# Kernel tuning notes

Hardware: AMD Instinct MI355X
Metric: run time of the kernel (lower is better)

## Reference

```python
import jax, jax.numpy as jnp
import numpy as np

N_NODES = 16384
N_EDGES = 262144
N_GRAPHS = 64
COLORS = 16
EMB = 256
HEADS = 8
FFN = 1024
LAYERS = 4
LMAX = 320


def _ln(x, g, b, eps=1e-5):
    m = x.mean(-1, keepdims=True)
    v = x.var(-1, keepdims=True)
    return (x - m) * jax.lax.rsqrt(v + eps) * g + b


def setup_inputs() -> dict:
    key = jax.random.key(0)
    ks = iter(jax.random.split(key, 64))
    s = 0.05
    def rn(shape):
        return jax.random.normal(next(ks), shape, jnp.float32) * s
    # 64 graphs: 32 with 192 nodes, 32 with 320 nodes -> total 16384, L_max=320
    lengths = np.concatenate([np.full(32, 192, np.int64), np.full(32, 320, np.int64)])
    batches = jnp.asarray(np.concatenate([[0], np.cumsum(lengths)]).astype(np.int32))
    x = jax.random.normal(next(ks), (N_NODES, COLORS), jnp.float32)
    edge_index = jax.random.randint(next(ks), (2, N_EDGES), 0, N_NODES, jnp.int32)
    inp = dict(
        x=x, edge_index=edge_index, batches=batches, L_max=LMAX,
        sW0=rn((COLORS, EMB)), sWn0=rn((COLORS, EMB)), sb0=jnp.zeros(EMB),
        sW1=rn((EMB, EMB)), sWn1=rn((EMB, EMB)), sb1=jnp.zeros(EMB),
        sW2=rn((EMB, EMB)), sWn2=rn((EMB, EMB)), sb2=jnp.zeros(EMB),
        Wq=rn((LAYERS, EMB, EMB)), Wk=rn((LAYERS, EMB, EMB)), Wv=rn((LAYERS, EMB, EMB)),
        bq=jnp.zeros((LAYERS, EMB)), bk=jnp.zeros((LAYERS, EMB)), bv=jnp.zeros((LAYERS, EMB)),
        Wo=rn((LAYERS, EMB, EMB)), bo=jnp.zeros((LAYERS, EMB)),
        ln1g=jnp.ones((LAYERS, EMB)), ln1b=jnp.zeros((LAYERS, EMB)),
        ln2g=jnp.ones((LAYERS, EMB)), ln2b=jnp.zeros((LAYERS, EMB)),
        W1=rn((LAYERS, EMB, FFN)), b1=jnp.zeros((LAYERS, FFN)),
        W2=rn((LAYERS, FFN, EMB)), b2=jnp.zeros((LAYERS, EMB)),
    )
    return inp


def reference(x, edge_index, batches, L_max,
              sW0, sWn0, sb0, sW1, sWn1, sb1, sW2, sWn2, sb2,
              Wq, Wk, Wv, bq, bk, bv, Wo, bo,
              ln1g, ln1b, ln2g, ln2b, W1, b1, W2, b2):
    N = x.shape[0]
    src, dst = edge_index[0], edge_index[1]
    deg = jnp.maximum(
        jax.ops.segment_sum(jnp.ones(src.shape[0], x.dtype), dst, num_segments=N), 1.0
    )[:, None]

    def sage(h, Ws, Wn, b, act):
        agg = jax.ops.segment_sum(h[src], dst, num_segments=N) / deg  # mean neighbor agg
        h2 = h @ Ws + agg @ Wn + b
        return jax.nn.relu(h2) if act else h2

    z = sage(x, sW0, sWn0, sb0, True)
    z = sage(z, sW1, sWn1, sb1, True)
    z = sage(z, sW2, sWn2, sb2, False)

    # pack_and_pad (intended semantics): seq-first [L_max, n_graphs, D] + key padding mask
    nG = batches.shape[0] - 1
    lengths = batches[1:] - batches[:-1]
    ids = jnp.arange(N)
    seg = jnp.searchsorted(batches, ids, side='right') - 1  # graph id per node
    pos = ids - batches[seg]                                 # position within graph
    D = z.shape[1]
    h = jnp.zeros((L_max, nG, D), z.dtype).at[pos, seg].set(z)
    pad = jnp.arange(L_max)[None, :] >= lengths[:, None]     # [nG, L_max], True = padded

    H = HEADS
    dh = D // H
    scale = 1.0 / np.sqrt(dh).astype(np.float32)
    for l in range(Wq.shape[0]):
        L, Bg = h.shape[0], h.shape[1]
        q = (h @ Wq[l] + bq[l]).reshape(L, Bg, H, dh)
        k = (h @ Wk[l] + bk[l]).reshape(L, Bg, H, dh)
        v = (h @ Wv[l] + bv[l]).reshape(L, Bg, H, dh)
        sc = jnp.einsum('lbhd,mbhd->bhlm', q, k) * scale
        sc = jnp.where(pad[:, None, None, :], -1e9, sc)
        a = jax.nn.softmax(sc, axis=-1)
        o = jnp.einsum('bhlm,mbhd->lbhd', a, v).reshape(L, Bg, D) @ Wo[l] + bo[l]
        h = _ln(h + o, ln1g[l], ln1b[l])
        ff = jax.nn.relu(h @ W1[l] + b1[l]) @ W2[l] + b2[l]
        h = _ln(h + ff, ln2g[l], ln2b[l])
    return h
```

## Files before the change

### kernel.cpp

```cpp
#include <hip/hip_runtime.h>
#include <hip/hip_bf16.h>
#include <math.h>

#define NN  16384
#define NE  262144
#define NG  64
#define CIN 16
#define DD  256
#define NHD 8
#define DHD 32
#define DFF 1024
#define NLY 4
#define LM  320
#define NR  (LM*NG)
#define QS  768
#define QKW 512

typedef __attribute__((ext_vector_type(8))) short bf16x8;
typedef __attribute__((ext_vector_type(4))) float f32x4;

__device__ __forceinline__ unsigned short f2bf(float f) {
    union { __hip_bfloat16 h; unsigned short u; } cv;
    cv.h = __float2bfloat16(f);
    return cv.u;
}
__device__ __forceinline__ float bf2f(unsigned short u) {
    return __uint_as_float((unsigned int)u << 16);
}
__device__ __forceinline__ void gl_lds16(const unsigned short* g, unsigned short* l) {
    __builtin_amdgcn_global_load_lds(
        (const __attribute__((address_space(1))) unsigned int*)g,
        (__attribute__((address_space(3))) unsigned int*)l, 16, 0, 0);
}

__global__ void zero_ws_kernel(uint4* __restrict__ hb, int n16, int* __restrict__ counts) {
    int i = blockIdx.x * 256 + threadIdx.x;
    if (i < n16) hb[i] = (uint4){0u, 0u, 0u, 0u};
    if (i < NN) counts[i] = 0;
}

__global__ __launch_bounds__(256) void prep_all_kernel(
    const float* __restrict__ Wq, const float* __restrict__ Wk, const float* __restrict__ Wv,
    const float* __restrict__ Wo, const float* __restrict__ W1, const float* __restrict__ W2,
    const float* __restrict__ sW1, const float* __restrict__ sWn1,
    const float* __restrict__ sW2, const float* __restrict__ sWn2,
    const float* __restrict__ bq, const float* __restrict__ bk, const float* __restrict__ bv,
    unsigned short* __restrict__ Wqkvt, unsigned short* __restrict__ Wot,
    unsigned short* __restrict__ W1t, unsigned short* __restrict__ W2t,
    unsigned short* __restrict__ sW1t, unsigned short* __restrict__ sWn1t,
    unsigned short* __restrict__ sW2t, unsigned short* __restrict__ sWn2t,
    float* __restrict__ bqkvp)
{
    const int t = threadIdx.x;
    int bid = blockIdx.x;
    if (bid < 12) {
        int i = bid * 256 + t;
        if (i < NLY * QS) {
            int n = i % QS, l = i / QS;
            const float* b = (n < 256) ? bq : (n < 512 ? bk : bv);
            float v = b[l * DD + (n & 255)];
            if (n < 256) v *= 0.17677669529663687f;
            bqkvp[i] = v;
        }
        return;
    }
    bid -= 12;
    __shared__ float Ls[64][68];
    const float* inP;
    unsigned short* outP;
    int strideIn, strideOut;
    float sc = 1.f;
    if (bid < 192) {
        int x = bid % 12, y = (bid / 12) % 4, l = bid / 48;
        int n0 = x * 64, k0 = y * 64;
        const float* W = (n0 < 256) ? Wq : (n0 < 512 ? Wk : Wv);
        if (n0 < 256) sc = 0.17677669529663687f;
        inP  = W + ((size_t)l * DD + k0) * DD + (n0 & 255);
        strideIn = DD;
        outP = Wqkvt + ((size_t)l * QS + n0) * DD + k0;
        strideOut = DD;
    } else if (bid < 192 + 64) {
        bid -= 192;
        int x = bid % 4, y = (bid / 4) % 4, l = bid / 16;
        int n0 = x * 64, k0 = y * 64;
        inP  = Wo + ((size_t)l * DD + k0) * DD + n0;
        strideIn = DD;
        outP = Wot + ((size_t)l * DD + n0) * DD + k0;
        strideOut = DD;
    } else if (bid < 192 + 64 + 256) {
        bid -= 192 + 64;
        int x = bid % 16, y = (bid / 16) % 4, l = bid / 64;
        int n0 = x * 64, k0 = y * 64;
        inP  = W1 + ((size_t)l * DD + k0) * DFF + n0;
        strideIn = DFF;
        outP = W1t + ((size_t)l * DFF + n0) * DD + k0;
        strideOut = DD;
    } else if (bid < 192 + 64 + 512) {
        bid -= 192 + 64 + 256;
        int x = bid % 4, y = (bid / 4) % 16, l = bid / 64;
        int n0 = x * 64, k0 = y * 64;
        inP  = W2 + ((size_t)l * DFF + k0) * DD + n0;
        strideIn = DD;
        outP = W2t + ((size_t)l * DD + n0) * DFF + k0;
        strideOut = DFF;
    } else {
        bid -= 192 + 64 + 512;
        int w = bid / 16, r = bid % 16;
        int x = r % 4, y = r / 4;
        int n0 = x * 64, k0 = y * 64;
        const float* src = (w == 0) ? sW1 : (w == 1) ? sWn1 : (w == 2) ? sW2 : sWn2;
        unsigned short* dst = (w == 0) ? sW1t : (w == 1) ? sWn1t : (w == 2) ? sW2t : sWn2t;
        inP  = src + (size_t)k0 * DD + n0;
        strideIn = DD;
        outP = dst + (size_t)n0 * DD + k0;
        strideOut = DD;
    }
    #pragma unroll
    for (int it = 0; it < 4; ++it) {
        int lin = it * 256 + t;
        int kr = lin >> 4, nc = (lin & 15) * 4;
        float4 v = *(const float4*)&inP[(size_t)kr * strideIn + nc];
        Ls[kr][nc]     = v.x * sc;
        Ls[kr][nc + 1] = v.y * sc;
        Ls[kr][nc + 2] = v.z * sc;
        Ls[kr][nc + 3] = v.w * sc;
    }
    __syncthreads();
    #pragma unroll
    for (int it = 0; it < 2; ++it) {
        int lin = it * 256 + t;
        int nr = lin >> 3, kc = (lin & 7) * 8;
        unsigned short pk[8];
        #pragma unroll
        for (int j = 0; j < 8; ++j) pk[j] = f2bf(Ls[kc + j][nr]);
        *(uint4*)&outP[(size_t)nr * strideOut + kc] = *(uint4*)pk;
    }
}

__global__ void count_edges_kernel(const int* __restrict__ dst, int* __restrict__ counts) {
    int e = blockIdx.x * 256 + threadIdx.x;
    if (e < NE) atomicAdd(&counts[dst[e]], 1);
}

__global__ __launch_bounds__(256) void scan_kernel(const int* __restrict__ counts,
                                                   int* __restrict__ offsets,
                                                   int* __restrict__ cursor) {
    __shared__ int part[256];
    int t = threadIdx.x;
    int base = t * 64;
    int s = 0;
    for (int i = 0; i < 64; ++i) s += counts[base + i];
    part[t] = s;
    __syncthreads();
    for (int off = 1; off < 256; off <<= 1) {
        int val = (t >= off) ? part[t - off] : 0;
        __syncthreads();
        part[t] += val;
        __syncthreads();
    }
    int run = (t == 0) ? 0 : part[t - 1];
    for (int i = 0; i < 64; ++i) {
        offsets[base + i] = run;
        cursor[base + i]  = run;
        run += counts[base + i];
    }
    if (t == 255) offsets[NN] = run;
}

__global__ void fill_csr_kernel(const int* __restrict__ src, const int* __restrict__ dst,
                                int* __restrict__ cursor, int* __restrict__ csr) {
    int e = blockIdx.x * 256 + threadIdx.x;
    if (e < NE) {
        int p = atomicAdd(&cursor[dst[e]], 1);
        csr[p] = src[e];
    }
}

__global__ __launch_bounds__(256) void agg_mean16_kernel(
    const float* __restrict__ h, const int* __restrict__ offsets,
    const int* __restrict__ csr, float* __restrict__ out)
{
    int node = blockIdx.x * 16 + (threadIdx.x >> 4);
    int d = threadIdx.x & 15;
    int beg = offsets[node], end = offsets[node + 1];
    float acc = 0.f;
    for (int e = beg; e < end; ++e) acc += h[(size_t)csr[e] * CIN + d];
    int dg = end - beg; if (dg < 1) dg = 1;
    out[(size_t)node * CIN + d] = acc * (1.f / (float)dg);
}

__global__ __launch_bounds__(256) void agg_mean_b_kernel(
    const unsigned short* __restrict__ h, const int* __restrict__ offsets,
    const int* __restrict__ csr, unsigned short* __restrict__ out)
{
    int node = blockIdx.x * 4 + (threadIdx.x >> 6);
    int lane = threadIdx.x & 63;
    int beg = offsets[node], end = offsets[node + 1];
    float a0 = 0.f, a1 = 0.f, a2 = 0.f, a3 = 0.f;
    for (int e = beg; e < end; ++e) {
        const ushort4 hv = *(const ushort4*)(h + (size_t)csr[e] * DD + lane * 4);
        a0 += bf2f(hv.x); a1 += bf2f(hv.y); a2 += bf2f(hv.z); a3 += bf2f(hv.w);
    }
    int dg = end - beg; if (dg < 1) dg = 1;
    float inv = 1.f / (float)dg;
    ushort4 ov;
    ov.x = f2bf(a0 * inv); ov.y = f2bf(a1 * inv);
    ov.z = f2bf(a2 * inv); ov.w = f2bf(a3 * inv);
    *(ushort4*)(out + (size_t)node * DD + lane * 4) = ov;
}

template <int ACT, bool DUAL>
__global__ __launch_bounds__(256) void gemm_f32b_kernel(
    const float* __restrict__ A, const float* __restrict__ W,
    const float* __restrict__ A2, const float* __restrict__ W2,
    const float* __restrict__ bias, unsigned short* __restrict__ Cb,
    int M, int N, int K)
{
    __shared__ __align__(16) float As[16][64];
    __shared__ __align__(16) float Ws[16][64];
    const int t  = threadIdx.x;
    const int tx = t & 15, ty = t >> 4;
    const int m0 = blockIdx.y * 64, n0 = blockIdx.x * 64;
    const int arow = t >> 2, acol = (t & 3) * 4;
    const int wrow = t >> 4, wcol = (t & 15) * 4;
    float acc[4][4] = {};
    const int npass = DUAL ? 2 : 1;
    for (int pass = 0; pass < npass; ++pass) {
        const float* Ap = (DUAL && pass) ? A2 : A;
        const float* Wp = (DUAL && pass) ? W2 : W;
        for (int k0 = 0; k0 < K; k0 += 16) {
            __syncthreads();
            float4 av = *(const float4*)(Ap + (size_t)(m0 + arow) * K + k0 + acol);
            As[acol + 0][arow] = av.x;
            As[acol + 1][arow] = av.y;
            As[acol + 2][arow] = av.z;
            As[acol + 3][arow] = av.w;
            *(float4*)&Ws[wrow][wcol] = *(const float4*)(Wp + (size_t)(k0 + wrow) * N + n0 + wcol);
            __syncthreads();
            #pragma unroll
            for (int kk = 0; kk < 16; ++kk) {
                float4 a4 = *(const float4*)&As[kk][ty * 4];
                float4 b4 = *(const float4*)&Ws[kk][tx * 4];
                float aa[4] = {a4.x, a4.y, a4.z, a4.w};
                float bb[4] = {b4.x, b4.y, b4.z, b4.w};
                #pragma unroll
                for (int i = 0; i < 4; ++i)
                    #pragma unroll
                    for (int j = 0; j < 4; ++j)
                        acc[i][j] += aa[i] * bb[j];
            }
        }
    }
    float4 bv = *(const float4*)(bias + n0 + tx * 4);
    float bb4[4] = {bv.x, bv.y, bv.z, bv.w};
    #pragma unroll
    for (int i = 0; i < 4; ++i) {
        float c[4];
        #pragma unroll
        for (int j = 0; j < 4; ++j) {
            c[j] = acc[i][j] + bb4[j];
            if (ACT == 1) c[j] = fmaxf(c[j], 0.f);
        }
        ushort4 ov;
        ov.x = f2bf(c[0]); ov.y = f2bf(c[1]); ov.z = f2bf(c[2]); ov.w = f2bf(c[3]);
        *(ushort4*)(Cb + (size_t)(m0 + ty * 4 + i) * N + n0 + tx * 4) = ov;
    }
}

template <int ACT, bool DUAL, bool OUTF32, bool OUTBF16>
__global__ __launch_bounds__(256) void mfma_gemm_kernel(
    const unsigned short* __restrict__ A,  const unsigned short* __restrict__ Wt,
    const unsigned short* __restrict__ A2, const unsigned short* __restrict__ Wt2,
    const float* __restrict__ bias, float* __restrict__ Cf,
    unsigned short* __restrict__ Cb, int M, int N, int K)
{
    __shared__ __align__(16) unsigned short As[128 * 32];
    __shared__ __align__(16) unsigned short Bs[128 * 32];
    const int t = threadIdx.x;
    const int wave = t >> 6, lane = t & 63;
    const int quad = lane >> 4, r16 = lane & 15;
    const int wr = (wave >> 1) * 64, wc = (wave & 1) * 64;
    const int m0 = blockIdx.y * 128, n0 = blockIdx.x * 128;
    const int srow = t >> 2, sq = (t & 3) * 8;

    unsigned short* la = As + wave * 512;
    unsigned short* lb = Bs + wave * 512;

    f32x4 acc[4][4];
    #pragma unroll
    for (int i = 0; i < 4; ++i)
        #pragma unroll
        for (int j = 0; j < 4; ++j)
            acc[i][j] = (f32x4){0.f, 0.f, 0.f, 0.f};

    const int npass = DUAL ? 2 : 1;
    for (int pass = 0; pass < npass; ++pass) {
        const unsigned short* Ap = (DUAL && pass) ? A2 : A;
        const unsigned short* Wp = (DUAL && pass) ? Wt2 : Wt;
        for (int k0 = 0; k0 < K; k0 += 32) {
            __syncthreads();
            gl_lds16(&Ap[(size_t)(m0 + srow) * K + k0 + sq],       la);
            gl_lds16(&Ap[(size_t)(m0 + 64 + srow) * K + k0 + sq],  la + 2048);
            gl_lds16(&Wp[(size_t)(n0 + srow) * K + k0 + sq],       lb);
            gl_lds16(&Wp[(size_t)(n0 + 64 + srow) * K + k0 + sq],  lb + 2048);
            __syncthreads();
            bf16x8 af[4], bfr[4];
            #pragma unroll
            for (int i = 0; i < 4; ++i)
                af[i] = *(const bf16x8*)&As[(wr + i * 16 + r16) * 32 + quad * 8];
            #pragma unroll
            for (int j = 0; j < 4; ++j)
                bfr[j] = *(const bf16x8*)&Bs[(wc + j * 16 + r16) * 32 + quad * 8];
            #pragma unroll
            for (int i = 0; i < 4; ++i)
                #pragma unroll
                for (int j = 0; j < 4; ++j)
                    acc[i][j] = __builtin_amdgcn_mfma_f32_16x16x32_bf16(
                        af[i], bfr[j], acc[i][j], 0, 0, 0);
        }
    }

    float bcol[4];
    #pragma unroll
    for (int j = 0; j < 4; ++j) bcol[j] = bias[n0 + wc + j * 16 + r16];
    #pragma unroll
    for (int i = 0; i < 4; ++i) {
        const int rowb = m0 + wr + i * 16 + quad * 4;
        #pragma unroll
        for (int rr = 0; rr < 4; ++rr) {
            const size_t rb = (size_t)(rowb + rr) * N;
            #pragma unroll
            for (int j = 0; j < 4; ++j) {
                float v = acc[i][j][rr] + bcol[j];
                if (ACT == 1) v = fmaxf(v, 0.f);
                const int col = n0 + wc + j * 16 + r16;
                if (OUTF32) Cf[rb + col] = v;
                if (OUTBF16) Cb[rb + col] = f2bf(v);
            }
        }
    }
}

__global__ __launch_bounds__(256) void gemm_qkv_kernel(
    const unsigned short* __restrict__ A, const unsigned short* __restrict__ Wt,
    const float* __restrict__ bias, unsigned short* __restrict__ QKb,
    unsigned short* __restrict__ Vt, int K)
{
    __shared__ __align__(16) unsigned short As[128 * 32];
    __shared__ __align__(16) unsigned short Bs[128 * 32];
    const int t = threadIdx.x;
    const int wave = t >> 6, lane = t & 63;
    const int quad = lane >> 4, r16 = lane & 15;
    const int wr = (wave >> 1) * 64, wc = (wave & 1) * 64;
    const int m0 = blockIdx.y * 128, n0 = blockIdx.x * 128;
    const int srow = t >> 2, sq = (t & 3) * 8;
    unsigned short* la = As + wave * 512;
    unsigned short* lb = Bs + wave * 512;

    f32x4 acc[4][4];
    #pragma unroll
    for (int i = 0; i < 4; ++i)
        #pragma unroll
        for (int j = 0; j < 4; ++j)
            acc[i][j] = (f32x4){0.f, 0.f, 0.f, 0.f};

    for (int k0 = 0; k0 < K; k0 += 32) {
        __syncthreads();
        gl_lds16(&A[(size_t)(m0 + srow) * K + k0 + sq],       la);
        gl_lds16(&A[(size_t)(m0 + 64 + srow) * K + k0 + sq],  la + 2048);
        gl_lds16(&Wt[(size_t)(n0 + srow) * K + k0 + sq],      lb);
        gl_lds16(&Wt[(size_t)(n0 + 64 + srow) * K + k0 + sq], lb + 2048);
        __syncthreads();
        bf16x8 af[4], bfr[4];
        #pragma unroll
        for (int i = 0; i < 4; ++i)
            af[i] = *(const bf16x8*)&As[(wr + i * 16 + r16) * 32 + quad * 8];
        #pragma unroll
        for (int j = 0; j < 4; ++j)
            bfr[j] = *(const bf16x8*)&Bs[(wc + j * 16 + r16) * 32 + quad * 8];
        #pragma unroll
        for (int i = 0; i < 4; ++i)
            #pragma unroll
            for (int j = 0; j < 4; ++j)
                acc[i][j] = __builtin_amdgcn_mfma_f32_16x16x32_bf16(
                    af[i], bfr[j], acc[i][j], 0, 0, 0);
    }

    float bcol[4];
    #pragma unroll
    for (int j = 0; j < 4; ++j) bcol[j] = bias[n0 + wc + j * 16 + r16];

    if (n0 < 512) {
        #pragma unroll
        for (int i = 0; i < 4; ++i) {
            const int rowb = m0 + wr + i * 16 + quad * 4;
            #pragma unroll
            for (int rr = 0; rr < 4; ++rr) {
                const size_t rb = (size_t)(rowb + rr) * QKW;
                #pragma unroll
                for (int j = 0; j < 4; ++j)
                    QKb[rb + n0 + wc + j * 16 + r16] = f2bf(acc[i][j][rr] + bcol[j]);
            }
        }
    } else {
        #pragma unroll
        for (int i = 0; i < 4; ++i) {
            const int rowb = m0 + wr + i * 16 + quad * 4;
            const int g = rowb / LM;
            const int key = rowb - g * LM;
            #pragma unroll
            for (int j = 0; j < 4; ++j) {
                const int dim = n0 - 512 + wc + j * 16 + r16;
                unsigned short pk[4];
                #pragma unroll
                for (int rr = 0; rr < 4; ++rr) pk[rr] = f2bf(acc[i][j][rr] + bcol[j]);
                *(uint2*)&Vt[((size_t)g * DD + dim) * LM + key] = *(uint2*)pk;
            }
        }
    }
}

template <bool PERM>
__global__ __launch_bounds__(256) void gemm_ln_kernel(
    const unsigned short* __restrict__ A, const unsigned short* __restrict__ Wt,
    const float* __restrict__ bias, const unsigned short* __restrict__ residb,
    const float* __restrict__ gam, const float* __restrict__ bet,
    float* __restrict__ outF, unsigned short* __restrict__ outHb, int K)
{
    __shared__ __align__(16) unsigned short As[32 * 32];
    __shared__ __align__(16) unsigned short Bs[256 * 32];
    __shared__ float red[2][4][32];
    const int t = threadIdx.x;
    const int wave = t >> 6, lane = t & 63;
    const int quad = lane >> 4, r16 = lane & 15;
    const int wc = wave * 64;
    const int m0 = blockIdx.x * 32;
    const int sr = lane >> 2, sq = (lane & 3) * 8;

    f32x4 acc[2][4];
    #pragma unroll
    for (int i = 0; i < 2; ++i)
        #pragma unroll
        for (int j = 0; j < 4; ++j)
            acc[i][j] = (f32x4){0.f, 0.f, 0.f, 0.f};

    for (int k0 = 0; k0 < K; k0 += 32) {
        __syncthreads();
        if (wave < 2)
            gl_lds16(&A[(size_t)(m0 + wave * 16 + sr) * K + k0 + sq], As + wave * 512);
        #pragma unroll
        for (int c = 0; c < 4; ++c)
            gl_lds16(&Wt[(size_t)(wc + c * 16 + sr) * K + k0 + sq],
                     Bs + wave * 2048 + c * 512);
        __syncthreads();
        bf16x8 af[2], bfr[4];
        #pragma unroll
        for (int i = 0; i < 2; ++i)
            af[i] = *(const bf16x8*)&As[(i * 16 + r16) * 32 + quad * 8];
        #pragma unroll
        for (int j = 0; j < 4; ++j)
            bfr[j] = *(const bf16x8*)&Bs[(wc + j * 16 + r16) * 32 + quad * 8];
        #pragma unroll
        for (int i = 0; i < 2; ++i)
            #pragma unroll
            for (int j = 0; j < 4; ++j)
                acc[i][j] = __builtin_amdgcn_mfma_f32_16x16x32_bf16(
                    af[i], bfr[j], acc[i][j], 0, 0, 0);
    }

    float bcol[4];
    #pragma unroll
    for (int j = 0; j < 4; ++j) bcol[j] = bias[wc + j * 16 + r16];

    #pragma unroll
    for (int i = 0; i < 2; ++i) {
        const int row = i * 16 + quad * 4;
        #pragma unroll
        for (int rr = 0; rr < 4; ++rr) {
            const size_t rb = (size_t)(m0 + row + rr) * DD;
            float s1 = 0.f, s2 = 0.f;
            #pragma unroll
            for (int j = 0; j < 4; ++j) {
                float v = acc[i][j][rr] + bcol[j] + bf2f(residb[rb + wc + j * 16 + r16]);
                acc[i][j][rr] = v;
                s1 += v;
                s2 += v * v;
            }
            #pragma unroll
            for (int off = 1; off < 16; off <<= 1) {
                s1 += __shfl_xor(s1, off, 64);
                s2 += __shfl_xor(s2, off, 64);
            }
            if (r16 == 0) {
                red[0][wave][row + rr] = s1;
                red[1][wave][row + rr] = s2;
            }
        }
    }
    __syncthreads();
    #pragma unroll
    for (int i = 0; i < 2; ++i) {
        const int row = i * 16 + quad * 4;
        #pragma unroll
        for (int rr = 0; rr < 4; ++rr) {
            const int gr = m0 + row + rr;
            float s1 = red[0][0][row + rr] + red[0][1][row + rr]
                     + red[0][2][row + rr] + red[0][3][row + rr];
            float s2 = red[1][0][row + rr] + red[1][1][row + rr]
                     + red[1][2][row + rr] + red[1][3][row + rr];
            float mean = s1 * (1.f / 256.f);
            float var  = s2 * (1.f / 256.f) - mean * mean;
            float rs = rsqrtf(var + 1e-5f);
            const size_t hb = (size_t)gr * DD;
            size_t fb = 0;
            if (PERM) {
                int gg = gr / LM, pos = gr - gg * LM;
                fb = ((size_t)pos * NG + gg) * DD;
            }
            #pragma unroll
            for (int j = 0; j < 4; ++j) {
                const int col = wc + j * 16 + r16;
                float ov = (acc[i][j][rr] - mean) * rs * gam[col] + bet[col];
                if (PERM) outF[fb + col] = ov;
                else      outHb[hb + col] = f2bf(ov);
            }
        }
    }
}

__global__ __launch_bounds__(256) void pack_kernel(
    const float* __restrict__ z, const int* __restrict__ batches,
    unsigned short* __restrict__ Hb)
{
    int node = blockIdx.x * 4 + (threadIdx.x >> 6);
    int lane = threadIdx.x & 63;
    int lo = 0, hi = NG;
    while (lo < hi) {
        int mid = (lo + hi + 1) >> 1;
        if (batches[mid] <= node) lo = mid; else hi = mid - 1;
    }
    int pos = node - batches[lo];
    size_t base = ((size_t)lo * LM + pos) * DD + lane * 4;
    float4 zv = *(const float4*)(z + (size_t)node * DD + lane * 4);
    ushort4 hb;
    hb.x = f2bf(zv.x); hb.y = f2bf(zv.y); hb.z = f2bf(zv.z); hb.w = f2bf(zv.w);
    *(ushort4*)(Hb + base) = hb;
}

__global__ __launch_bounds__(256) void attn_mfma_kernel(
    const unsigned short* __restrict__ qk, const unsigned short* __restrict__ vt,
    const int* __restrict__ batches, unsigned short* __restrict__ o)
{
    __shared__ __align__(16) unsigned short Pa[4][32 * 40];
    const int bx = blockIdx.x;
    const int g = bx & 63;
    const int r = bx >> 6;
    const int q0 = (r >> 1) * 32;
    const int tid = threadIdx.x;
    const int wave = tid >> 6;
    const int h = (r & 1) * 4 + wave;
    const int lane = tid & 63;
    const int quad = lane >> 4, r16 = lane & 15;
    const int len = batches[g + 1] - batches[g];
    const size_t gq = (size_t)g * LM;
    unsigned short* pa = Pa[wave];

    bf16x8 qf[2];
    #pragma unroll
    for (int i = 0; i < 2; ++i)
        qf[i] = *(const bf16x8*)(qk + (gq + q0 + i * 16 + r16) * QKW + h * 32 + quad * 8);
    bf16x8 onesf;
    #pragma unroll
    for (int j = 0; j < 8; ++j) onesf[j] = (short)0x3F80;

    f32x4 oacc[2][2], lacc[2];
    #pragma unroll
    for (int i = 0; i < 2; ++i) {
        lacc[i] = (f32x4){0.f, 0.f, 0.f, 0.f};
        #pragma unroll
        for (int nt = 0; nt < 2; ++nt)
            oacc[i][nt] = (f32x4){0.f, 0.f, 0.f, 0.f};
    }

    for (int t0 = 0; t0 < len; t0 += 32) {
        bf16x8 kf[2], vf[2];
        #pragma unroll
        for (int mt = 0; mt < 2; ++mt) {
            int kr = t0 + mt * 16 + r16; if (kr > LM - 1) kr = LM - 1;
            kf[mt] = *(const bf16x8*)(qk + (gq + kr) * QKW + 256 + h * 32 + quad * 8);
        }
        #pragma unroll
        for (int nt = 0; nt < 2; ++nt)
            vf[nt] = *(const bf16x8*)(vt + ((size_t)g * DD + h * 32 + nt * 16 + r16) * LM
                                      + t0 + quad * 8);
        f32x4 st[2][2];
        #pragma unroll
        for (int mt = 0; mt < 2; ++mt)
            #pragma unroll
            for (int i = 0; i < 2; ++i)
                st[mt][i] = (f32x4){0.f, 0.f, 0.f, 0.f};
        #pragma unroll
        for (int mt = 0; mt < 2; ++mt)
            #pragma unroll
            for (int i = 0; i < 2; ++i)
                st[mt][i] = __builtin_amdgcn_mfma_f32_16x16x32_bf16(
                    kf[mt], qf[i], st[mt][i], 0, 0, 0);
        #pragma unroll
        for (int i = 0; i < 2; ++i) {
            #pragma unroll
            for (int mt = 0; mt < 2; ++mt) {
                float pr[4];
                #pragma unroll
                for (int rr = 0; rr < 4; ++rr) {
                    int key = t0 + mt * 16 + quad * 4 + rr;
                    pr[rr] = (key < len) ? __expf(st[mt][i][rr]) : 0.f;
                }
                uint2 w;
                w.x = ((unsigned)f2bf(pr[1]) << 16) | f2bf(pr[0]);
                w.y = ((unsigned)f2bf(pr[3]) << 16) | f2bf(pr[2]);
                *(uint2*)&pa[(i * 16 + r16) * 40 + mt * 16 + quad * 4] = w;
            }
        }
        __asm__ volatile("s_waitcnt lgkmcnt(0)" ::: "memory");
        bf16x8 pf[2];
        #pragma unroll
        for (int i = 0; i < 2; ++i)
            pf[i] = *(const bf16x8*)&pa[(i * 16 + r16) * 40 + quad * 8];
        #pragma unroll
        for (int i = 0; i < 2; ++i) {
            #pragma unroll
            for (int nt = 0; nt < 2; ++nt)
                oacc[i][nt] = __builtin_amdgcn_mfma_f32_16x16x32_bf16(
                    pf[i], vf[nt], oacc[i][nt], 0, 0, 0);
            lacc[i] = __builtin_amdgcn_mfma_f32_16x16x32_bf16(
                pf[i], onesf, lacc[i], 0, 0, 0);
        }
    }
    #pragma unroll
    for (int i = 0; i < 2; ++i) {
        #pragma unroll
        for (int rr = 0; rr < 4; ++rr) {
            float inv = 1.f / lacc[i][rr];
            size_t base = (gq + q0 + i * 16 + quad * 4 + rr) * DD + h * 32;
            #pragma unroll
            for (int nt = 0; nt < 2; ++nt)
                o[base + nt * 16 + r16] = f2bf(oacc[i][nt][rr] * inv);
        }
    }
}

extern "C" void kernel_launch(void* const* d_in, const int* in_sizes, int n_in,
                              void* d_out, int out_size, void* d_ws, size_t ws_size,
                              hipStream_t stream) {
    const float* x       = (const float*)d_in[0];
    const int*   ei      = (const int*)d_in[1];
    const int*   batches = (const int*)d_in[2];
    const float* sW0  = (const float*)d_in[4];
    const float* sWn0 = (const float*)d_in[5];
    const float* sb0  = (const float*)d_in[6];
    const float* sW1  = (const float*)d_in[7];
    const float* sWn1 = (const float*)d_in[8];
    const float* sb1  = (const float*)d_in[9];
    const float* sW2  = (const float*)d_in[10];
    const float* sWn2 = (const float*)d_in[11];
    const float* sb2  = (const float*)d_in[12];
    const float* Wq   = (const float*)d_in[13];
    const float* Wk   = (const float*)d_in[14];
    const float* Wv   = (const float*)d_in[15];
    const float* bq   = (const float*)d_in[16];
    const float* bk   = (const float*)d_in[17];
    const float* bv   = (const float*)d_in[18];
    const float* Wo   = (const float*)d_in[19];
    const float* bo   = (const float*)d_in[20];
    const float* ln1g = (const float*)d_in[21];
    const float* ln1b = (const float*)d_in[22];
    const float* ln2g = (const float*)d_in[23];
    const float* ln2b = (const float*)d_in[24];
    const float* W1   = (const float*)d_in[25];
    const float* b1   = (const float*)d_in[26];
    const float* W2   = (const float*)d_in[27];
    const float* b2   = (const float*)d_in[28];

    char* p = (char*)d_ws;
    auto alloc = [&](size_t bytes) {
        char* r = p;
        p += (bytes + 255) & ~(size_t)255;
        return r;
    };
    int*   counts  = (int*)alloc((size_t)NN * 4);
    int*   offsets = (int*)alloc((size_t)(NN + 1) * 4);
    int*   cursor  = (int*)alloc((size_t)NN * 4);
    int*   csr     = (int*)alloc((size_t)NE * 4);
    float* agg0    = (float*)alloc((size_t)NN * CIN * 4);
    unsigned short* z0b = (unsigned short*)alloc((size_t)NN * DD * 2);
    unsigned short* a1b = (unsigned short*)alloc((size_t)NN * DD * 2);
    unsigned short* z1b = (unsigned short*)alloc((size_t)NN * DD * 2);
    unsigned short* a2b = (unsigned short*)alloc((size_t)NN * DD * 2);
    float* z2f     = (float*)alloc((size_t)NN * DD * 4);
    unsigned short* Vt = (unsigned short*)z2f;
    unsigned short* Hb = (unsigned short*)alloc((size_t)NR * DD * 2);
    unsigned short* Ob = (unsigned short*)alloc((size_t)NR * DD * 2);
    float* R       = (float*)alloc((size_t)NR * DFF * 2);
    unsigned short* QKb = (unsigned short*)R;
    unsigned short* F1b = (unsigned short*)R;
    unsigned short* Wqkvt = (unsigned short*)alloc((size_t)NLY * QS * DD * 2);
    unsigned short* Wot   = (unsigned short*)alloc((size_t)NLY * DD * DD * 2);
    unsigned short* W1t   = (unsigned short*)alloc((size_t)NLY * DFF * DD * 2);
    unsigned short* W2t   = (unsigned short*)alloc((size_t)NLY * DD * DFF * 2);
    unsigned short* sW1t  = (unsigned short*)alloc((size_t)DD * DD * 2);
    unsigned short* sWn1t = (unsigned short*)alloc((size_t)DD * DD * 2);
    unsigned short* sW2t  = (unsigned short*)alloc((size_t)DD * DD * 2);
    unsigned short* sWn2t = (unsigned short*)alloc((size_t)DD * DD * 2);
    float* bqkvp   = (float*)alloc((size_t)NLY * QS * 4);

    prep_all_kernel<<<844, 256, 0, stream>>>(
        Wq, Wk, Wv, Wo, W1, W2, sW1, sWn1, sW2, sWn2, bq, bk, bv,
        Wqkvt, Wot, W1t, W2t, sW1t, sWn1t, sW2t, sWn2t, bqkvp);
    zero_ws_kernel<<<(NR * DD / 8 + 255) / 256, 256, 0, stream>>>(
        (uint4*)Hb, NR * DD / 8, counts);

    count_edges_kernel<<<NE / 256, 256, 0, stream>>>(ei + NE, counts);
    scan_kernel<<<1, 256, 0, stream>>>(counts, offsets, cursor);
    fill_csr_kernel<<<NE / 256, 256, 0, stream>>>(ei, ei + NE, cursor, csr);

    agg_mean16_kernel<<<NN / 16, 256, 0, stream>>>(x, offsets, csr, agg0);
    gemm_f32b_kernel<1, true><<<dim3(DD / 64, NN / 64), 256, 0, stream>>>(
        x, sW0, agg0, sWn0, sb0, z0b, NN, DD, CIN);
    agg_mean_b_kernel<<<NN / 4, 256, 0, stream>>>(z0b, offsets, csr, a1b);
    mfma_gemm_kernel<1, true, false, true><<<dim3(DD / 128, NN / 128), 256, 0, stream>>>(
        z0b, sW1t, a1b, sWn1t, sb1, nullptr, z1b, NN, DD, DD);
    agg_mean_b_kernel<<<NN / 4, 256, 0, stream>>>(z1b, offsets, csr, a2b);
    mfma_gemm_kernel<0, true, true, false><<<dim3(DD / 128, NN / 128), 256, 0, stream>>>(
        z1b, sW2t, a2b, sWn2t, sb2, z2f, nullptr, NN, DD, DD);

    pack_kernel<<<NN / 4, 256, 0, stream>>>(z2f, batches, Hb);

    for (int l = 0; l < NLY; ++l) {
        gemm_qkv_kernel<<<dim3(QS / 128, NR / 128), 256, 0, stream>>>(
            Hb, Wqkvt + (size_t)l * QS * DD, bqkvp + (size_t)l * QS, QKb, Vt, DD);
        attn_mfma_kernel<<<NG * 20, 256, 0, stream>>>(QKb, Vt, batches, Ob);
        gemm_ln_kernel<false><<<NR / 32, 256, 0, stream>>>(
            Ob, Wot + (size_t)l * DD * DD, bo + (size_t)l * DD, Hb,
            ln1g + (size_t)l * DD, ln1b + (size_t)l * DD, nullptr, Hb, DD);
        mfma_gemm_kernel<1, false, false, true><<<dim3(DFF / 128, NR / 128), 256, 0, stream>>>(
            Hb, W1t + (size_t)l * DFF * DD, nullptr, nullptr,
            b1 + (size_t)l * DFF, nullptr, F1b, NR, DFF, DD);
        if (l == NLY - 1)
            gemm_ln_kernel<true><<<NR / 32, 256, 0, stream>>>(
                F1b, W2t + (size_t)l * DD * DFF, b2 + (size_t)l * DD, Hb,
                ln2g + (size_t)l * DD, ln2b + (size_t)l * DD, (float*)d_out, Hb, DFF);
        else
            gemm_ln_kernel<false><<<NR / 32, 256, 0, stream>>>(
                F1b, W2t + (size_t)l * DD * DFF, b2 + (size_t)l * DD, Hb,
                ln2g + (size_t)l * DD, ln2b + (size_t)l * DD, nullptr, Hb, DFF);
    }
}
```

Measured before the change: 806.2 us.

## Enlarge row tiles in GEMM-LN and attention kernels, widen CSR scan

The GEMM+LayerNorm kernel now processes 64 rows per block with 8 waves, so each weight tile staged in shared memory is reused by twice as many rows. The attention kernel handles 64 queries per wave instead of 32, so each K/V fragment load serves more query tiles, and the grid is halved to match. The CSR scan uses 1024 threads with 16 elements each, which shortens each thread's serial part. The cost is higher register and LDS use per block and fewer blocks in flight, which may lower occupancy and latency hiding.

```diff
diff --git a/kernel.cpp b/kernel.cpp
--- a/kernel.cpp
+++ b/kernel.cpp
@@ -142,29 +142,31 @@
     if (e < NE) atomicAdd(&counts[dst[e]], 1);
 }
 
-__global__ __launch_bounds__(256) void scan_kernel(const int* __restrict__ counts,
-                                                   int* __restrict__ offsets,
-                                                   int* __restrict__ cursor) {
-    __shared__ int part[256];
+__global__ __launch_bounds__(1024) void scan_kernel(const int* __restrict__ counts,
+                                                    int* __restrict__ offsets,
+                                                    int* __restrict__ cursor) {
+    __shared__ int part[1024];
     int t = threadIdx.x;
-    int base = t * 64;
+    int base = t * 16;
     int s = 0;
-    for (int i = 0; i < 64; ++i) s += counts[base + i];
+    #pragma unroll
+    for (int i = 0; i < 16; ++i) s += counts[base + i];
     part[t] = s;
     __syncthreads();
-    for (int off = 1; off < 256; off <<= 1) {
+    for (int off = 1; off < 1024; off <<= 1) {
         int val = (t >= off) ? part[t - off] : 0;
         __syncthreads();
         part[t] += val;
         __syncthreads();
     }
     int run = (t == 0) ? 0 : part[t - 1];
-    for (int i = 0; i < 64; ++i) {
+    #pragma unroll
+    for (int i = 0; i < 16; ++i) {
         offsets[base + i] = run;
         cursor[base + i]  = run;
         run += counts[base + i];
     }
-    if (t == 255) offsets[NN] = run;
+    if (t == 1023) offsets[NN] = run;
 }
 
 __global__ void fill_csr_kernel(const int* __restrict__ src, const int* __restrict__ dst,
@@ -421,21 +423,22 @@
 }
 
 template <bool PERM>
-__global__ __launch_bounds__(256) void gemm_ln_kernel(
+__global__ __launch_bounds__(512) void gemm_ln_kernel(
     const unsigned short* __restrict__ A, const unsigned short* __restrict__ Wt,
     const float* __restrict__ bias, const unsigned short* __restrict__ residb,
     const float* __restrict__ gam, const float* __restrict__ bet,
     float* __restrict__ outF, unsigned short* __restrict__ outHb, int K)
 {
-    __shared__ __align__(16) unsigned short As[32 * 32];
+    __shared__ __align__(16) unsigned short As[64 * 32];
     __shared__ __align__(16) unsigned short Bs[256 * 32];
-    __shared__ float red[2][4][32];
+    __shared__ float red[2][4][64];
     const int t = threadIdx.x;
     const int wave = t >> 6, lane = t & 63;
     const int quad = lane >> 4, r16 = lane & 15;
-    const int wc = wave * 64;
-    const int m0 = blockIdx.x * 32;
-    const int sr = lane >> 2, sq = (lane & 3) * 8;
+    const int wr = (wave >> 2) * 32;
+    const int wc = (wave & 3) * 64;
+    const int m0 = blockIdx.x * 64;
+    const int srow = t >> 2, sq = (t & 3) * 8;
 
     f32x4 acc[2][4];
     #pragma unroll
@@ -446,17 +449,15 @@
 
     for (int k0 = 0; k0 < K; k0 += 32) {
         __syncthreads();
-        if (wave < 2)
-            gl_lds16(&A[(size_t)(m0 + wave * 16 + sr) * K + k0 + sq], As + wave * 512);
-        #pragma unroll
-        for (int c = 0; c < 4; ++c)
-            gl_lds16(&Wt[(size_t)(wc + c * 16 + sr) * K + k0 + sq],
-                     Bs + wave * 2048 + c * 512);
+        if (wave < 4)
+            gl_lds16(&A[(size_t)(m0 + srow) * K + k0 + sq], As + wave * 512);
+        gl_lds16(&Wt[(size_t)srow * K + k0 + sq],         Bs + wave * 512);
+        gl_lds16(&Wt[(size_t)(128 + srow) * K + k0 + sq], Bs + 4096 + wave * 512);
         __syncthreads();
         bf16x8 af[2], bfr[4];
         #pragma unroll
         for (int i = 0; i < 2; ++i)
-            af[i] = *(const bf16x8*)&As[(i * 16 + r16) * 32 + quad * 8];
+            af[i] = *(const bf16x8*)&As[(wr + i * 16 + r16) * 32 + quad * 8];
         #pragma unroll
         for (int j = 0; j < 4; ++j)
             bfr[j] = *(const bf16x8*)&Bs[(wc + j * 16 + r16) * 32 + quad * 8];
@@ -474,7 +475,7 @@
 
     #pragma unroll
     for (int i = 0; i < 2; ++i) {
-        const int row = i * 16 + quad * 4;
+        const int row = wr + i * 16 + quad * 4;
         #pragma unroll
         for (int rr = 0; rr < 4; ++rr) {
             const size_t rb = (size_t)(m0 + row + rr) * DD;
@@ -492,22 +493,21 @@
                 s2 += __shfl_xor(s2, off, 64);
             }
             if (r16 == 0) {
-                red[0][wave][row + rr] = s1;
-                red[1][wave][row + rr] = s2;
+                red[0][wave & 3][row + rr] = s1;
+                red[1][wave & 3][row + rr] = s2;
             }
         }
     }
     __syncthreads();
     #pragma unroll
     for (int i = 0; i < 2; ++i) {
-        const int row = i * 16 + quad * 4;
+        const int row = wr + i * 16 + quad * 4;
         #pragma unroll
         for (int rr = 0; rr < 4; ++rr) {
-            const int gr = m0 + row + rr;
-            float s1 = red[0][0][row + rr] + red[0][1][row + rr]
-                     + red[0][2][row + rr] + red[0][3][row + rr];
-            float s2 = red[1][0][row + rr] + red[1][1][row + rr]
-                     + red[1][2][row + rr] + red[1][3][row + rr];
+            const int lr = row + rr;
+            const int gr = m0 + lr;
+            float s1 = red[0][0][lr] + red[0][1][lr] + red[0][2][lr] + red[0][3][lr];
+            float s2 = red[1][0][lr] + red[1][1][lr] + red[1][2][lr] + red[1][3][lr];
             float mean = s1 * (1.f / 256.f);
             float var  = s2 * (1.f / 256.f) - mean * mean;
             float rs = rsqrtf(var + 1e-5f);
@@ -551,11 +551,11 @@
     const unsigned short* __restrict__ qk, const unsigned short* __restrict__ vt,
     const int* __restrict__ batches, unsigned short* __restrict__ o)
 {
-    __shared__ __align__(16) unsigned short Pa[4][32 * 40];
+    __shared__ __align__(16) unsigned short Pa[4][64 * 40];
     const int bx = blockIdx.x;
     const int g = bx & 63;
     const int r = bx >> 6;
-    const int q0 = (r >> 1) * 32;
+    const int q0 = (r >> 1) * 64;
     const int tid = threadIdx.x;
     const int wave = tid >> 6;
     const int h = (r & 1) * 4 + wave;
@@ -565,17 +565,17 @@
     const size_t gq = (size_t)g * LM;
     unsigned short* pa = Pa[wave];
 
-    bf16x8 qf[2];
-    #pragma unroll
-    for (int i = 0; i < 2; ++i)
+    bf16x8 qf[4];
+    #pragma unroll
+    for (int i = 0; i < 4; ++i)
         qf[i] = *(const bf16x8*)(qk + (gq + q0 + i * 16 + r16) * QKW + h * 32 + quad * 8);
     bf16x8 onesf;
     #pragma unroll
     for (int j = 0; j < 8; ++j) onesf[j] = (short)0x3F80;
 
-    f32x4 oacc[2][2], lacc[2];
-    #pragma unroll
-    for (int i = 0; i < 2; ++i) {
+    f32x4 oacc[4][2], lacc[4];
+    #pragma unroll
+    for (int i = 0; i < 4; ++i) {
         lacc[i] = (f32x4){0.f, 0.f, 0.f, 0.f};
         #pragma unroll
         for (int nt = 0; nt < 2; ++nt)
@@ -593,20 +593,20 @@
         for (int nt = 0; nt < 2; ++nt)
             vf[nt] = *(const bf16x8*)(vt + ((size_t)g * DD + h * 32 + nt * 16 + r16) * LM
                                       + t0 + quad * 8);
-        f32x4 st[2][2];
+        f32x4 st[2][4];
         #pragma unroll
         for (int mt = 0; mt < 2; ++mt)
             #pragma unroll
-            for (int i = 0; i < 2; ++i)
+            for (int i = 0; i < 4; ++i)
                 st[mt][i] = (f32x4){0.f, 0.f, 0.f, 0.f};
         #pragma unroll
         for (int mt = 0; mt < 2; ++mt)
             #pragma unroll
-            for (int i = 0; i < 2; ++i)
+            for (int i = 0; i < 4; ++i)
                 st[mt][i] = __builtin_amdgcn_mfma_f32_16x16x32_bf16(
                     kf[mt], qf[i], st[mt][i], 0, 0, 0);
         #pragma unroll
-        for (int i = 0; i < 2; ++i) {
+        for (int i = 0; i < 4; ++i) {
             #pragma unroll
             for (int mt = 0; mt < 2; ++mt) {
                 float pr[4];
@@ -622,12 +622,12 @@
             }
         }
         __asm__ volatile("s_waitcnt lgkmcnt(0)" ::: "memory");
-        bf16x8 pf[2];
-        #pragma unroll
-        for (int i = 0; i < 2; ++i)
+        bf16x8 pf[4];
+        #pragma unroll
+        for (int i = 0; i < 4; ++i)
             pf[i] = *(const bf16x8*)&pa[(i * 16 + r16) * 40 + quad * 8];
         #pragma unroll
-        for (int i = 0; i < 2; ++i) {
+        for (int i = 0; i < 4; ++i) {
             #pragma unroll
             for (int nt = 0; nt < 2; ++nt)
                 oacc[i][nt] = __builtin_amdgcn_mfma_f32_16x16x32_bf16(
@@ -637,7 +637,7 @@
         }
     }
     #pragma unroll
-    for (int i = 0; i < 2; ++i) {
+    for (int i = 0; i < 4; ++i) {
         #pragma unroll
         for (int rr = 0; rr < 4; ++rr) {
             float inv = 1.f / lacc[i][rr];
@@ -720,7 +720,7 @@
         (uint4*)Hb, NR * DD / 8, counts);
 
     count_edges_kernel<<<NE / 256, 256, 0, stream>>>(ei + NE, counts);
-    scan_kernel<<<1, 256, 0, stream>>>(counts, offsets, cursor);
+    scan_kernel<<<1, 1024, 0, stream>>>(counts, offsets, cursor);
     fill_csr_kernel<<<NE / 256, 256, 0, stream>>>(ei, ei + NE, cursor, csr);
 
     agg_mean16_kernel<<<NN / 16, 256, 0, stream>>>(x, offsets, csr, agg0);
@@ -738,19 +738,19 @@
     for (int l = 0; l < NLY; ++l) {
         gemm_qkv_kernel<<<dim3(QS / 128, NR / 128), 256, 0, stream>>>(
             Hb, Wqkvt + (size_t)l * QS * DD, bqkvp + (size_t)l * QS, QKb, Vt, DD);
-        attn_mfma_kernel<<<NG * 20, 256, 0, stream>>>(QKb, Vt, batches, Ob);
-        gemm_ln_kernel<false><<<NR / 32, 256, 0, stream>>>(
+        attn_mfma_kernel<<<NG * 10, 256, 0, stream>>>(QKb, Vt, batches, Ob);
+        gemm_ln_kernel<false><<<NR / 64, 512, 0, stream>>>(
             Ob, Wot + (size_t)l * DD * DD, bo + (size_t)l * DD, Hb,
             ln1g + (size_t)l * DD, ln1b + (size_t)l * DD, nullptr, Hb, DD);
         mfma_gemm_kernel<1, false, false, true><<<dim3(DFF / 128, NR / 128), 256, 0, stream>>>(
             Hb, W1t + (size_t)l * DFF * DD, nullptr, nullptr,
             b1 + (size_t)l * DFF, nullptr, F1b, NR, DFF, DD);
         if (l == NLY - 1)
-            gemm_ln_kernel<true><<<NR / 32, 256, 0, stream>>>(
+            gemm_ln_kernel<true><<<NR / 64, 512, 0, stream>>>(
                 F1b, W2t + (size_t)l * DD * DFF, b2 + (size_t)l * DD, Hb,
                 ln2g + (size_t)l * DD, ln2b + (size_t)l * DD, (float*)d_out, Hb, DFF);
         else
-            gemm_ln_kernel<false><<<NR / 32, 256, 0, stream>>>(
+            gemm_ln_kernel<false><<<NR / 64, 512, 0, stream>>>(
                 F1b, W2t + (size_t)l * DD * DFF, b2 + (size_t)l * DD, Hb,
                 ln2g + (size_t)l * DD, ln2b + (size_t)l * DD, nullptr, Hb, DFF);
     }
```

Result: faster. 785.6 us (-2.5%).
